# Performance work log

Measured on AMD Instinct MI355X. Metric: run time of the kernel, lower is better.

The kernel has to match this reference:

```python
import jax, jax.numpy as jnp
import numpy as np

DVEC = 128
B, S = 4, 1024


def setup_inputs() -> dict:
    key = jax.random.key(0)
    k1, k2 = jax.random.split(key)
    func_and_arg = jax.random.normal(k1, (B, S, 2 * DVEC), dtype=jnp.float32)
    cooccurrences = jax.random.normal(k2, (DVEC, DVEC, DVEC), dtype=jnp.float32)
    return {"func_and_arg": func_and_arg, "cooccurrences": cooccurrences}


def reference(func_and_arg, cooccurrences):
    # out[b,s,z] = sum_{i,j} func[b,s,i] * cooc[i,j,z] * arg[b,s,j]
    d = cooccurrences.shape[0]
    func = func_and_arg[..., :d]   # [B,S,D]
    arg = func_and_arg[..., d:]    # [B,S,D]
    # contract func over i first -> [B,S,D(j),Z], then arg over j -> [B,S,Z]
    tmp = jnp.einsum('bsi,ijz->bsjz', func, cooccurrences)
    return jnp.einsum('bsjz,bsj->bsz', tmp, arg)
```

## Files before the change

### kernel.cpp

```cpp
#include <hip/hip_runtime.h>
#include <hip/hip_bf16.h>


typedef __attribute__((ext_vector_type(8))) short bf16x8;
typedef __attribute__((ext_vector_type(4))) float f32x4;

__device__ __forceinline__ unsigned pkbf16(float x, float y) {
    __hip_bfloat162 h = __float22bfloat162_rn(make_float2(x, y));
    unsigned u; __builtin_memcpy(&u, &h, sizeof(u));
    return u;
}

__global__ __launch_bounds__(256) void cooc_transpose(
    const float* __restrict__ Cc, ushort* __restrict__ CT)
{
    __shared__ float tile[32][132];
    const int i  = blockIdx.x >> 2;
    const int j0 = (blockIdx.x & 3) * 32;
    const int t  = threadIdx.x;
    {
        const int jj = t >> 3;
        const int zb = (t & 7) * 16;
        const float* src = Cc + (size_t)i * 16384 + (size_t)(j0 + jj) * 128 + zb;
        #pragma unroll
        for (int k = 0; k < 4; ++k)
            *(float4*)&tile[jj][zb + k * 4] = *(const float4*)(src + k * 4);
    }
    __syncthreads();
    {
        const int z = t >> 1;
        const int h = t & 1;
        unsigned o[8];
        #pragma unroll
        for (int p = 0; p < 8; ++p)
            o[p] = pkbf16(tile[h * 16 + 2 * p][z], tile[h * 16 + 2 * p + 1][z]);
        const int c0 = (j0 >> 3) + h * 2;
        ushort* dst = CT + (size_t)i * 16384 + (size_t)(z >> 4) * 2048
                         + (size_t)c0 * 128 + (z & 15) * 8;
        *(uint4*)dst         = make_uint4(o[0], o[1], o[2], o[3]);
        *(uint4*)(dst + 128) = make_uint4(o[4], o[5], o[6], o[7]);
    }
}

__global__ __launch_bounds__(256) void cooc_apack(
    const float* __restrict__ fa, ushort* __restrict__ APK)
{
    const int g = blockIdx.x;
    const int t = threadIdx.x;
    const int ks = t >> 6, lk = (t >> 4) & 3, lm = t & 15;
    const float* src = fa + (size_t)(g * 16 + lm) * 256 + 128 + ks * 32 + lk * 8;
    float4 q0 = *(const float4*)src;
    float4 q1 = *(const float4*)(src + 4);
    unsigned o0 = pkbf16(q0.x, q0.y), o1 = pkbf16(q0.z, q0.w);
    unsigned o2 = pkbf16(q1.x, q1.y), o3 = pkbf16(q1.z, q1.w);
    *(uint4*)(APK + (size_t)g * 2048 + t * 8) = make_uint4(o0, o1, o2, o3);
}

template<int USE_WS>
__global__ __launch_bounds__(256, 3) void cooc_main(
    const float* __restrict__ fa, const ushort* __restrict__ CT,
    const ushort* __restrict__ APK, float* __restrict__ dst)
{
    __shared__ float f_lds[16][128];

    const int bid = blockIdx.x;
    const int kp = bid & 7, zp = (bid >> 3) & 3, mtile = bid >> 5;
    const int t0 = mtile * 128, i0 = kp * 16;
    const int tid = threadIdx.x, lane = tid & 63, wv = tid >> 6;
    const int mg = wv >> 1, zg = wv & 1;
    const int lm = lane & 15, lk = lane >> 4;

    {
        const int row = tid & 127;
        const int sh = (tid >> 7) * 8;
        const float* fp = fa + (size_t)(t0 + row) * 256 + i0 + sh;
        float4 v0 = *(const float4*)fp;
        float4 v1 = *(const float4*)(fp + 4);
        f_lds[sh + 0][row] = v0.x; f_lds[sh + 1][row] = v0.y;
        f_lds[sh + 2][row] = v0.z; f_lds[sh + 3][row] = v0.w;
        f_lds[sh + 4][row] = v1.x; f_lds[sh + 5][row] = v1.y;
        f_lds[sh + 6][row] = v1.z; f_lds[sh + 7][row] = v1.w;
    }

    bf16x8 a_pk[4][4];
    {
        const ushort* ap = APK + (size_t)((t0 >> 4) + mg * 4) * 2048 + lane * 8;
        #pragma unroll
        for (int m = 0; m < 4; ++m)
            #pragma unroll
            for (int ks = 0; ks < 4; ++ks)
                a_pk[m][ks] = *(const bf16x8*)(ap + (size_t)m * 2048 + ks * 512);
    }
    __syncthreads();

    const ushort* bsrc = CT + (size_t)i0 * 16384
                            + (size_t)(zp * 2 + zg) * 2048 + lane * 8;

    bf16x8 B[2][4];
    #pragma unroll
    for (int ks = 0; ks < 4; ++ks) {
        B[0][ks] = *(const bf16x8*)(bsrc + ks * 512);
        B[1][ks] = *(const bf16x8*)(bsrc + 16384 + ks * 512);
    }

    float acc[4][4];
    #pragma unroll
    for (int m = 0; m < 4; ++m)
        #pragma unroll
        for (int r = 0; r < 4; ++r) acc[m][r] = 0.f;

    #pragma unroll 2
    for (int s = 0; s < 16; ++s) {
        const int cur = s & 1;

        f32x4 g[4];
        #pragma unroll
        for (int m = 0; m < 4; ++m) g[m] = (f32x4){0.f, 0.f, 0.f, 0.f};
        #pragma unroll
        for (int ks = 0; ks < 4; ++ks)
            #pragma unroll
            for (int m = 0; m < 4; ++m)
                g[m] = __builtin_amdgcn_mfma_f32_16x16x32_bf16(
                    a_pk[m][ks], B[cur][ks], g[m], 0, 0, 0);

        if (s < 14) {
            const ushort* p = bsrc + (size_t)(s + 2) * 16384;
            #pragma unroll
            for (int ks = 0; ks < 4; ++ks)
                B[cur][ks] = *(const bf16x8*)(p + ks * 512);
        }

        float4 f4[4];
        #pragma unroll
        for (int m = 0; m < 4; ++m)
            f4[m] = *(const float4*)&f_lds[s][mg * 64 + m * 16 + lk * 4];
        #pragma unroll
        for (int m = 0; m < 4; ++m) {
            acc[m][0] += f4[m].x * g[m][0];
            acc[m][1] += f4[m].y * g[m][1];
            acc[m][2] += f4[m].z * g[m][2];
            acc[m][3] += f4[m].w * g[m][3];
        }
    }

    const int col = zp * 32 + zg * 16 + lm;
    #pragma unroll
    for (int m = 0; m < 4; ++m)
        #pragma unroll
        for (int r = 0; r < 4; ++r) {
            const int row = t0 + mg * 64 + m * 16 + lk * 4 + r;
            if (USE_WS)
                dst[(size_t)kp * 524288 + (size_t)row * 128 + col] = acc[m][r];
            else
                atomicAdd(&dst[(size_t)row * 128 + col], acc[m][r]);
        }
}

__global__ __launch_bounds__(256) void cooc_reduce(const float* __restrict__ ws,
                                                   float* __restrict__ out) {
    const size_t idx = ((size_t)blockIdx.x * 256 + threadIdx.x) * 4;
    float4 a = *(const float4*)(ws + idx);
    #pragma unroll
    for (int k = 1; k < 8; ++k) {
        float4 b = *(const float4*)(ws + (size_t)k * 524288 + idx);
        a.x += b.x; a.y += b.y; a.z += b.z; a.w += b.w;
    }
    *(float4*)(out + idx) = a;
}

extern "C" void kernel_launch(void* const* d_in, const int* in_sizes, int n_in,
                              void* d_out, int out_size, void* d_ws, size_t ws_size,
                              hipStream_t stream) {
    const float* fa = (const float*)d_in[0];
    const float* Cc = (const float*)d_in[1];
    float* out = (float*)d_out;

    const size_t PART = (size_t)8 * 524288;
    const size_t CTOF = PART * sizeof(float);
    const size_t CTSZ = (size_t)128 * 128 * 128 * 2;
    const size_t APOF = CTOF + CTSZ;
    const size_t APSZ = (size_t)4096 * 128 * 2;
    const size_t NEED_FULL = APOF + APSZ;
    const size_t NEED_CT   = CTSZ + APSZ;

    if (ws_size >= NEED_FULL) {
        ushort* CT  = (ushort*)((char*)d_ws + CTOF);
        ushort* APK = (ushort*)((char*)d_ws + APOF);
        cooc_transpose<<<512, 256, 0, stream>>>(Cc, CT);
        cooc_apack<<<256, 256, 0, stream>>>(fa, APK);
        cooc_main<1><<<1024, 256, 0, stream>>>(fa, CT, APK, (float*)d_ws);
        cooc_reduce<<<512, 256, 0, stream>>>((const float*)d_ws, out);
    } else if (ws_size >= NEED_CT) {
        ushort* CT  = (ushort*)d_ws;
        ushort* APK = (ushort*)((char*)d_ws + CTSZ);
        cooc_transpose<<<512, 256, 0, stream>>>(Cc, CT);
        cooc_apack<<<256, 256, 0, stream>>>(fa, APK);
        (void)hipMemsetAsync(out, 0, (size_t)out_size * sizeof(float), stream);
        cooc_main<0><<<1024, 256, 0, stream>>>(fa, CT, APK, out);
    } else {
        (void)hipMemsetAsync(out, 0, (size_t)out_size * sizeof(float), stream);
        cooc_main<0><<<1024, 256, 0, stream>>>(fa, (const ushort*)d_ws,
                                               (const ushort*)d_ws, out);
    }
}
```

Baseline: 86.22 us.

## Merge prep kernels and share cooccurrence B tiles through LDS across waves

The transpose and activation-pack kernels become a single launch, dropping one kernel launch. In the main kernel each wave now loads only half of its B chunk from global memory and the waves exchange the halves through a double-buffered LDS tile, so the two wave pairs that use the same B stop fetching it twice. The func values are stored in LDS as bf16, which halves their footprint. The cost is a __syncthreads in every iteration, extra LDS traffic, and extra rounding of func to bf16.

```diff
diff --git a/kernel.cpp b/kernel.cpp
--- a/kernel.cpp
+++ b/kernel.cpp
@@ -10,50 +10,55 @@
     unsigned u; __builtin_memcpy(&u, &h, sizeof(u));
     return u;
 }
-
-__global__ __launch_bounds__(256) void cooc_transpose(
-    const float* __restrict__ Cc, ushort* __restrict__ CT)
+__device__ __forceinline__ float bf16lo(unsigned u) {
+    unsigned v = u << 16; float f; __builtin_memcpy(&f, &v, 4); return f;
+}
+__device__ __forceinline__ float bf16hi(unsigned u) {
+    unsigned v = u & 0xFFFF0000u; float f; __builtin_memcpy(&f, &v, 4); return f;
+}
+
+__global__ __launch_bounds__(256) void cooc_prep(
+    const float* __restrict__ Cc, const float* __restrict__ fa,
+    ushort* __restrict__ CT, ushort* __restrict__ APK)
 {
-    __shared__ float tile[32][132];
-    const int i  = blockIdx.x >> 2;
-    const int j0 = (blockIdx.x & 3) * 32;
-    const int t  = threadIdx.x;
-    {
-        const int jj = t >> 3;
-        const int zb = (t & 7) * 16;
-        const float* src = Cc + (size_t)i * 16384 + (size_t)(j0 + jj) * 128 + zb;
-        #pragma unroll
-        for (int k = 0; k < 4; ++k)
-            *(float4*)&tile[jj][zb + k * 4] = *(const float4*)(src + k * 4);
-    }
-    __syncthreads();
-    {
-        const int z = t >> 1;
-        const int h = t & 1;
-        unsigned o[8];
-        #pragma unroll
-        for (int p = 0; p < 8; ++p)
-            o[p] = pkbf16(tile[h * 16 + 2 * p][z], tile[h * 16 + 2 * p + 1][z]);
-        const int c0 = (j0 >> 3) + h * 2;
-        ushort* dst = CT + (size_t)i * 16384 + (size_t)(z >> 4) * 2048
-                         + (size_t)c0 * 128 + (z & 15) * 8;
-        *(uint4*)dst         = make_uint4(o[0], o[1], o[2], o[3]);
-        *(uint4*)(dst + 128) = make_uint4(o[4], o[5], o[6], o[7]);
-    }
-}
-
-__global__ __launch_bounds__(256) void cooc_apack(
-    const float* __restrict__ fa, ushort* __restrict__ APK)
-{
-    const int g = blockIdx.x;
+    const int bid = blockIdx.x;
     const int t = threadIdx.x;
-    const int ks = t >> 6, lk = (t >> 4) & 3, lm = t & 15;
-    const float* src = fa + (size_t)(g * 16 + lm) * 256 + 128 + ks * 32 + lk * 8;
-    float4 q0 = *(const float4*)src;
-    float4 q1 = *(const float4*)(src + 4);
-    unsigned o0 = pkbf16(q0.x, q0.y), o1 = pkbf16(q0.z, q0.w);
-    unsigned o2 = pkbf16(q1.x, q1.y), o3 = pkbf16(q1.z, q1.w);
-    *(uint4*)(APK + (size_t)g * 2048 + t * 8) = make_uint4(o0, o1, o2, o3);
+    if (bid < 512) {
+        __shared__ float tile[32][132];
+        const int i  = bid >> 2;
+        const int j0 = (bid & 3) * 32;
+        {
+            const int jj = t >> 3;
+            const int zb = (t & 7) * 16;
+            const float* src = Cc + (size_t)i * 16384 + (size_t)(j0 + jj) * 128 + zb;
+            #pragma unroll
+            for (int k = 0; k < 4; ++k)
+                *(float4*)&tile[jj][zb + k * 4] = *(const float4*)(src + k * 4);
+        }
+        __syncthreads();
+        {
+            const int z = t >> 1;
+            const int h = t & 1;
+            unsigned o[8];
+            #pragma unroll
+            for (int p = 0; p < 8; ++p)
+                o[p] = pkbf16(tile[h * 16 + 2 * p][z], tile[h * 16 + 2 * p + 1][z]);
+            const int c0 = (j0 >> 3) + h * 2;
+            ushort* dst = CT + (size_t)i * 16384 + (size_t)(z >> 4) * 2048
+                             + (size_t)c0 * 128 + (z & 15) * 8;
+            *(uint4*)dst         = make_uint4(o[0], o[1], o[2], o[3]);
+            *(uint4*)(dst + 128) = make_uint4(o[4], o[5], o[6], o[7]);
+        }
+    } else {
+        const int g = bid - 512;
+        const int ks = t >> 6, lk = (t >> 4) & 3, lm = t & 15;
+        const float* src = fa + (size_t)(g * 16 + lm) * 256 + 128 + ks * 32 + lk * 8;
+        float4 q0 = *(const float4*)src;
+        float4 q1 = *(const float4*)(src + 4);
+        *(uint4*)(APK + (size_t)g * 2048 + t * 8) =
+            make_uint4(pkbf16(q0.x, q0.y), pkbf16(q0.z, q0.w),
+                       pkbf16(q1.x, q1.y), pkbf16(q1.z, q1.w));
+    }
 }
 
 template<int USE_WS>
@@ -61,7 +66,8 @@
     const float* __restrict__ fa, const ushort* __restrict__ CT,
     const ushort* __restrict__ APK, float* __restrict__ dst)
 {
-    __shared__ float f_lds[16][128];
+    __shared__ ushort Bbuf[2][2][4][512];
+    __shared__ ushort fpk[16][128];
 
     const int bid = blockIdx.x;
     const int kp = bid & 7, zp = (bid >> 3) & 3, mtile = bid >> 5;
@@ -76,10 +82,14 @@
         const float* fp = fa + (size_t)(t0 + row) * 256 + i0 + sh;
         float4 v0 = *(const float4*)fp;
         float4 v1 = *(const float4*)(fp + 4);
-        f_lds[sh + 0][row] = v0.x; f_lds[sh + 1][row] = v0.y;
-        f_lds[sh + 2][row] = v0.z; f_lds[sh + 3][row] = v0.w;
-        f_lds[sh + 4][row] = v1.x; f_lds[sh + 5][row] = v1.y;
-        f_lds[sh + 6][row] = v1.z; f_lds[sh + 7][row] = v1.w;
+        fpk[sh + 0][row] = (ushort)(pkbf16(v0.x, v0.x) & 0xFFFF);
+        fpk[sh + 1][row] = (ushort)(pkbf16(v0.y, v0.y) & 0xFFFF);
+        fpk[sh + 2][row] = (ushort)(pkbf16(v0.z, v0.z) & 0xFFFF);
+        fpk[sh + 3][row] = (ushort)(pkbf16(v0.w, v0.w) & 0xFFFF);
+        fpk[sh + 4][row] = (ushort)(pkbf16(v1.x, v1.x) & 0xFFFF);
+        fpk[sh + 5][row] = (ushort)(pkbf16(v1.y, v1.y) & 0xFFFF);
+        fpk[sh + 6][row] = (ushort)(pkbf16(v1.z, v1.z) & 0xFFFF);
+        fpk[sh + 7][row] = (ushort)(pkbf16(v1.w, v1.w) & 0xFFFF);
     }
 
     bf16x8 a_pk[4][4];
@@ -91,17 +101,21 @@
             for (int ks = 0; ks < 4; ++ks)
                 a_pk[m][ks] = *(const bf16x8*)(ap + (size_t)m * 2048 + ks * 512);
     }
+
+    const ushort* bchunk = CT + (size_t)i0 * 16384
+                              + (size_t)(zp * 2 + zg) * 2048
+                              + (size_t)(2 * mg) * 512 + lane * 8;
+
+    bf16x8 Bg[2][2];
+    #pragma unroll
+    for (int c = 0; c < 2; ++c) {
+        Bg[0][c] = *(const bf16x8*)(bchunk + c * 512);
+        Bg[1][c] = *(const bf16x8*)(bchunk + 16384 + c * 512);
+    }
+    #pragma unroll
+    for (int c = 0; c < 2; ++c)
+        *(bf16x8*)&Bbuf[0][zg][2 * mg + c][lane * 8] = Bg[0][c];
     __syncthreads();
-
-    const ushort* bsrc = CT + (size_t)i0 * 16384
-                            + (size_t)(zp * 2 + zg) * 2048 + lane * 8;
-
-    bf16x8 B[2][4];
-    #pragma unroll
-    for (int ks = 0; ks < 4; ++ks) {
-        B[0][ks] = *(const bf16x8*)(bsrc + ks * 512);
-        B[1][ks] = *(const bf16x8*)(bsrc + 16384 + ks * 512);
-    }
 
     float acc[4][4];
     #pragma unroll
@@ -113,6 +127,28 @@
     for (int s = 0; s < 16; ++s) {
         const int cur = s & 1;
 
+        if (s < 15)
+            #pragma unroll
+            for (int c = 0; c < 2; ++c)
+                *(bf16x8*)&Bbuf[cur ^ 1][zg][2 * mg + c][lane * 8] = Bg[cur ^ 1][c];
+
+        if (s < 14) {
+            const ushort* p = bchunk + (size_t)(s + 2) * 16384;
+            #pragma unroll
+            for (int c = 0; c < 2; ++c)
+                Bg[cur][c] = *(const bf16x8*)(p + c * 512);
+        }
+
+        bf16x8 Bl[4];
+        #pragma unroll
+        for (int ks = 0; ks < 4; ++ks)
+            Bl[ks] = *(const bf16x8*)&Bbuf[cur][zg][ks][lane * 8];
+
+        uint2 fq[4];
+        #pragma unroll
+        for (int m = 0; m < 4; ++m)
+            fq[m] = *(const uint2*)&fpk[s][mg * 64 + m * 16 + lk * 4];
+
         f32x4 g[4];
         #pragma unroll
         for (int m = 0; m < 4; ++m) g[m] = (f32x4){0.f, 0.f, 0.f, 0.f};
@@ -121,26 +157,17 @@
             #pragma unroll
             for (int m = 0; m < 4; ++m)
                 g[m] = __builtin_amdgcn_mfma_f32_16x16x32_bf16(
-                    a_pk[m][ks], B[cur][ks], g[m], 0, 0, 0);
-
-        if (s < 14) {
-            const ushort* p = bsrc + (size_t)(s + 2) * 16384;
-            #pragma unroll
-            for (int ks = 0; ks < 4; ++ks)
-                B[cur][ks] = *(const bf16x8*)(p + ks * 512);
-        }
-
-        float4 f4[4];
-        #pragma unroll
-        for (int m = 0; m < 4; ++m)
-            f4[m] = *(const float4*)&f_lds[s][mg * 64 + m * 16 + lk * 4];
+                    a_pk[m][ks], Bl[ks], g[m], 0, 0, 0);
+
         #pragma unroll
         for (int m = 0; m < 4; ++m) {
-            acc[m][0] += f4[m].x * g[m][0];
-            acc[m][1] += f4[m].y * g[m][1];
-            acc[m][2] += f4[m].z * g[m][2];
-            acc[m][3] += f4[m].w * g[m][3];
-        }
+            acc[m][0] += bf16lo(fq[m].x) * g[m][0];
+            acc[m][1] += bf16hi(fq[m].x) * g[m][1];
+            acc[m][2] += bf16lo(fq[m].y) * g[m][2];
+            acc[m][3] += bf16hi(fq[m].y) * g[m][3];
+        }
+
+        __syncthreads();
     }
 
     const int col = zp * 32 + zg * 16 + lm;
@@ -186,15 +213,13 @@
     if (ws_size >= NEED_FULL) {
         ushort* CT  = (ushort*)((char*)d_ws + CTOF);
         ushort* APK = (ushort*)((char*)d_ws + APOF);
-        cooc_transpose<<<512, 256, 0, stream>>>(Cc, CT);
-        cooc_apack<<<256, 256, 0, stream>>>(fa, APK);
+        cooc_prep<<<768, 256, 0, stream>>>(Cc, fa, CT, APK);
         cooc_main<1><<<1024, 256, 0, stream>>>(fa, CT, APK, (float*)d_ws);
         cooc_reduce<<<512, 256, 0, stream>>>((const float*)d_ws, out);
     } else if (ws_size >= NEED_CT) {
         ushort* CT  = (ushort*)d_ws;
         ushort* APK = (ushort*)((char*)d_ws + CTSZ);
-        cooc_transpose<<<512, 256, 0, stream>>>(Cc, CT);
-        cooc_apack<<<256, 256, 0, stream>>>(fa, APK);
+        cooc_prep<<<768, 256, 0, stream>>>(Cc, fa, CT, APK);
         (void)hipMemsetAsync(out, 0, (size_t)out_size * sizeof(float), stream);
         cooc_main<0><<<1024, 256, 0, stream>>>(fa, CT, APK, out);
     } else {
```

After: 86.18 us. No clear change (-0.0%).

## Merge prep kernels and halve main-kernel M tile to double grid size

Applied to the files above, without the earlier changes.

Folds the cooc transpose and A-packing kernels into one launch, with the work chosen by block index, which removes one kernel launch. The main kernel's row tile drops from 128 to 64, so the grid doubles to 2048 blocks, the register and LDS footprint per block shrinks, and the occupancy hint rises from 3 to 4 blocks. In exchange, each B tile loaded from CT now feeds half as many MFMAs, so the CT operand is re-read twice as often across the grid. The a_pk array also gains a redundant copy that is never read.

```diff
diff --git a/kernel.cpp b/kernel.cpp
--- a/kernel.cpp
+++ b/kernel.cpp
@@ -11,85 +11,85 @@
     return u;
 }
 
-__global__ __launch_bounds__(256) void cooc_transpose(
-    const float* __restrict__ Cc, ushort* __restrict__ CT)
+__global__ __launch_bounds__(256) void cooc_prep(
+    const float* __restrict__ Cc, const float* __restrict__ fa,
+    ushort* __restrict__ CT, ushort* __restrict__ APK)
 {
-    __shared__ float tile[32][132];
-    const int i  = blockIdx.x >> 2;
-    const int j0 = (blockIdx.x & 3) * 32;
-    const int t  = threadIdx.x;
-    {
-        const int jj = t >> 3;
-        const int zb = (t & 7) * 16;
-        const float* src = Cc + (size_t)i * 16384 + (size_t)(j0 + jj) * 128 + zb;
-        #pragma unroll
-        for (int k = 0; k < 4; ++k)
-            *(float4*)&tile[jj][zb + k * 4] = *(const float4*)(src + k * 4);
-    }
-    __syncthreads();
-    {
-        const int z = t >> 1;
-        const int h = t & 1;
-        unsigned o[8];
-        #pragma unroll
-        for (int p = 0; p < 8; ++p)
-            o[p] = pkbf16(tile[h * 16 + 2 * p][z], tile[h * 16 + 2 * p + 1][z]);
-        const int c0 = (j0 >> 3) + h * 2;
-        ushort* dst = CT + (size_t)i * 16384 + (size_t)(z >> 4) * 2048
-                         + (size_t)c0 * 128 + (z & 15) * 8;
-        *(uint4*)dst         = make_uint4(o[0], o[1], o[2], o[3]);
-        *(uint4*)(dst + 128) = make_uint4(o[4], o[5], o[6], o[7]);
-    }
-}
-
-__global__ __launch_bounds__(256) void cooc_apack(
-    const float* __restrict__ fa, ushort* __restrict__ APK)
-{
-    const int g = blockIdx.x;
+    const int bid = blockIdx.x;
     const int t = threadIdx.x;
-    const int ks = t >> 6, lk = (t >> 4) & 3, lm = t & 15;
-    const float* src = fa + (size_t)(g * 16 + lm) * 256 + 128 + ks * 32 + lk * 8;
-    float4 q0 = *(const float4*)src;
-    float4 q1 = *(const float4*)(src + 4);
-    unsigned o0 = pkbf16(q0.x, q0.y), o1 = pkbf16(q0.z, q0.w);
-    unsigned o2 = pkbf16(q1.x, q1.y), o3 = pkbf16(q1.z, q1.w);
-    *(uint4*)(APK + (size_t)g * 2048 + t * 8) = make_uint4(o0, o1, o2, o3);
+    if (bid < 512) {
+        __shared__ float tile[32][132];
+        const int i  = bid >> 2;
+        const int j0 = (bid & 3) * 32;
+        {
+            const int jj = t >> 3;
+            const int zb = (t & 7) * 16;
+            const float* src = Cc + (size_t)i * 16384 + (size_t)(j0 + jj) * 128 + zb;
+            #pragma unroll
+            for (int k = 0; k < 4; ++k)
+                *(float4*)&tile[jj][zb + k * 4] = *(const float4*)(src + k * 4);
+        }
+        __syncthreads();
+        {
+            const int z = t >> 1;
+            const int h = t & 1;
+            unsigned o[8];
+            #pragma unroll
+            for (int p = 0; p < 8; ++p)
+                o[p] = pkbf16(tile[h * 16 + 2 * p][z], tile[h * 16 + 2 * p + 1][z]);
+            const int c0 = (j0 >> 3) + h * 2;
+            ushort* dst = CT + (size_t)i * 16384 + (size_t)(z >> 4) * 2048
+                             + (size_t)c0 * 128 + (z & 15) * 8;
+            *(uint4*)dst         = make_uint4(o[0], o[1], o[2], o[3]);
+            *(uint4*)(dst + 128) = make_uint4(o[4], o[5], o[6], o[7]);
+        }
+    } else {
+        const int g = bid - 512;
+        const int ks = t >> 6, lk = (t >> 4) & 3, lm = t & 15;
+        const float* src = fa + (size_t)(g * 16 + lm) * 256 + 128 + ks * 32 + lk * 8;
+        float4 q0 = *(const float4*)src;
+        float4 q1 = *(const float4*)(src + 4);
+        *(uint4*)(APK + (size_t)g * 2048 + t * 8) =
+            make_uint4(pkbf16(q0.x, q0.y), pkbf16(q0.z, q0.w),
+                       pkbf16(q1.x, q1.y), pkbf16(q1.z, q1.w));
+    }
 }
 
 template<int USE_WS>
-__global__ __launch_bounds__(256, 3) void cooc_main(
+__global__ __launch_bounds__(256, 4) void cooc_main(
     const float* __restrict__ fa, const ushort* __restrict__ CT,
     const ushort* __restrict__ APK, float* __restrict__ dst)
 {
-    __shared__ float f_lds[16][128];
+    __shared__ float f_lds[16][64];
 
     const int bid = blockIdx.x;
     const int kp = bid & 7, zp = (bid >> 3) & 3, mtile = bid >> 5;
-    const int t0 = mtile * 128, i0 = kp * 16;
+    const int t0 = mtile * 64, i0 = kp * 16;
     const int tid = threadIdx.x, lane = tid & 63, wv = tid >> 6;
     const int mg = wv >> 1, zg = wv & 1;
     const int lm = lane & 15, lk = lane >> 4;
 
     {
-        const int row = tid & 127;
-        const int sh = (tid >> 7) * 8;
+        const int row = tid & 63;
+        const int sh = (tid >> 6) * 4;
         const float* fp = fa + (size_t)(t0 + row) * 256 + i0 + sh;
-        float4 v0 = *(const float4*)fp;
-        float4 v1 = *(const float4*)(fp + 4);
-        f_lds[sh + 0][row] = v0.x; f_lds[sh + 1][row] = v0.y;
-        f_lds[sh + 2][row] = v0.z; f_lds[sh + 3][row] = v0.w;
-        f_lds[sh + 4][row] = v1.x; f_lds[sh + 5][row] = v1.y;
-        f_lds[sh + 6][row] = v1.z; f_lds[sh + 7][row] = v1.w;
-    }
-
-    bf16x8 a_pk[4][4];
+        float4 v = *(const float4*)fp;
+        f_lds[sh + 0][row] = v.x;
+        f_lds[sh + 1][row] = v.y;
+        f_lds[sh + 2][row] = v.z;
+        f_lds[sh + 3][row] = v.w;
+    }
+
+    bf16x8 a_pk[2][2][4];
     {
-        const ushort* ap = APK + (size_t)((t0 >> 4) + mg * 4) * 2048 + lane * 8;
-        #pragma unroll
-        for (int m = 0; m < 4; ++m)
-            #pragma unroll
-            for (int ks = 0; ks < 4; ++ks)
-                a_pk[m][ks] = *(const bf16x8*)(ap + (size_t)m * 2048 + ks * 512);
+        const ushort* ap = APK + (size_t)((t0 >> 4) + mg * 2) * 2048 + lane * 8;
+        #pragma unroll
+        for (int m = 0; m < 2; ++m)
+            #pragma unroll
+            for (int ks = 0; ks < 4; ++ks) {
+                a_pk[0][m][ks] = *(const bf16x8*)(ap + (size_t)m * 2048 + ks * 512);
+                a_pk[1][m][ks] = a_pk[0][m][ks];
+            }
     }
     __syncthreads();
 
@@ -103,9 +103,9 @@
         B[1][ks] = *(const bf16x8*)(bsrc + 16384 + ks * 512);
     }
 
-    float acc[4][4];
-    #pragma unroll
-    for (int m = 0; m < 4; ++m)
+    float acc[2][4];
+    #pragma unroll
+    for (int m = 0; m < 2; ++m)
         #pragma unroll
         for (int r = 0; r < 4; ++r) acc[m][r] = 0.f;
 
@@ -113,15 +113,16 @@
     for (int s = 0; s < 16; ++s) {
         const int cur = s & 1;
 
-        f32x4 g[4];
-        #pragma unroll
-        for (int m = 0; m < 4; ++m) g[m] = (f32x4){0.f, 0.f, 0.f, 0.f};
-        #pragma unroll
-        for (int ks = 0; ks < 4; ++ks)
-            #pragma unroll
-            for (int m = 0; m < 4; ++m)
-                g[m] = __builtin_amdgcn_mfma_f32_16x16x32_bf16(
-                    a_pk[m][ks], B[cur][ks], g[m], 0, 0, 0);
+        f32x4 g[2];
+        g[0] = (f32x4){0.f, 0.f, 0.f, 0.f};
+        g[1] = (f32x4){0.f, 0.f, 0.f, 0.f};
+        #pragma unroll
+        for (int ks = 0; ks < 4; ++ks) {
+            g[0] = __builtin_amdgcn_mfma_f32_16x16x32_bf16(
+                a_pk[0][0][ks], B[cur][ks], g[0], 0, 0, 0);
+            g[1] = __builtin_amdgcn_mfma_f32_16x16x32_bf16(
+                a_pk[0][1][ks], B[cur][ks], g[1], 0, 0, 0);
+        }
 
         if (s < 14) {
             const ushort* p = bsrc + (size_t)(s + 2) * 16384;
@@ -130,12 +131,11 @@
                 B[cur][ks] = *(const bf16x8*)(p + ks * 512);
         }
 
-        float4 f4[4];
-        #pragma unroll
-        for (int m = 0; m < 4; ++m)
-            f4[m] = *(const float4*)&f_lds[s][mg * 64 + m * 16 + lk * 4];
-        #pragma unroll
-        for (int m = 0; m < 4; ++m) {
+        float4 f4[2];
+        f4[0] = *(const float4*)&f_lds[s][mg * 32 + lk * 4];
+        f4[1] = *(const float4*)&f_lds[s][mg * 32 + 16 + lk * 4];
+        #pragma unroll
+        for (int m = 0; m < 2; ++m) {
             acc[m][0] += f4[m].x * g[m][0];
             acc[m][1] += f4[m].y * g[m][1];
             acc[m][2] += f4[m].z * g[m][2];
@@ -145,10 +145,10 @@
 
     const int col = zp * 32 + zg * 16 + lm;
     #pragma unroll
-    for (int m = 0; m < 4; ++m)
+    for (int m = 0; m < 2; ++m)
         #pragma unroll
         for (int r = 0; r < 4; ++r) {
-            const int row = t0 + mg * 64 + m * 16 + lk * 4 + r;
+            const int row = t0 + mg * 32 + m * 16 + lk * 4 + r;
             if (USE_WS)
                 dst[(size_t)kp * 524288 + (size_t)row * 128 + col] = acc[m][r];
             else
@@ -186,20 +186,18 @@
     if (ws_size >= NEED_FULL) {
         ushort* CT  = (ushort*)((char*)d_ws + CTOF);
         ushort* APK = (ushort*)((char*)d_ws + APOF);
-        cooc_transpose<<<512, 256, 0, stream>>>(Cc, CT);
-        cooc_apack<<<256, 256, 0, stream>>>(fa, APK);
-        cooc_main<1><<<1024, 256, 0, stream>>>(fa, CT, APK, (float*)d_ws);
+        cooc_prep<<<768, 256, 0, stream>>>(Cc, fa, CT, APK);
+        cooc_main<1><<<2048, 256, 0, stream>>>(fa, CT, APK, (float*)d_ws);
         cooc_reduce<<<512, 256, 0, stream>>>((const float*)d_ws, out);
     } else if (ws_size >= NEED_CT) {
         ushort* CT  = (ushort*)d_ws;
         ushort* APK = (ushort*)((char*)d_ws + CTSZ);
-        cooc_transpose<<<512, 256, 0, stream>>>(Cc, CT);
-        cooc_apack<<<256, 256, 0, stream>>>(fa, APK);
+        cooc_prep<<<768, 256, 0, stream>>>(Cc, fa, CT, APK);
         (void)hipMemsetAsync(out, 0, (size_t)out_size * sizeof(float), stream);
-        cooc_main<0><<<1024, 256, 0, stream>>>(fa, CT, APK, out);
+        cooc_main<0><<<2048, 256, 0, stream>>>(fa, CT, APK, out);
     } else {
         (void)hipMemsetAsync(out, 0, (size_t)out_size * sizeof(float), stream);
-        cooc_main<0><<<1024, 256, 0, stream>>>(fa, (const ushort*)d_ws,
+        cooc_main<0><<<2048, 256, 0, stream>>>(fa, (const ushort*)d_ws,
                                                (const ushort*)d_ws, out);
     }
 }
```

Measured after the change: 89.00 us. 1.03x slower.

## Fuse prep kernels and output zeroing, replace workspace reduction with atomics

Applied to the files above, without the earlier changes.

Merges the bf16 transpose of the cooccurrence tensor, the arg packing, and zeroing of the output into one launch. The main kernel now always accumulates its 8 K-split partials with atomicAdd, which removes the partial-sum workspace and the separate reduce kernel. The aim is fewer kernel launches and less workspace traffic, at the cost of atomic contention on the output and a non-deterministic summation order. A naive fp32 fallback replaces the old path for a too-small workspace.

```diff
diff --git a/kernel.cpp b/kernel.cpp
--- a/kernel.cpp
+++ b/kernel.cpp
@@ -11,55 +11,60 @@
     return u;
 }
 
-__global__ __launch_bounds__(256) void cooc_transpose(
-    const float* __restrict__ Cc, ushort* __restrict__ CT)
+__global__ __launch_bounds__(256) void cooc_prep(
+    const float* __restrict__ Cc, const float* __restrict__ fa,
+    ushort* __restrict__ CT, ushort* __restrict__ APK, float* __restrict__ out)
 {
-    __shared__ float tile[32][132];
-    const int i  = blockIdx.x >> 2;
-    const int j0 = (blockIdx.x & 3) * 32;
-    const int t  = threadIdx.x;
-    {
-        const int jj = t >> 3;
-        const int zb = (t & 7) * 16;
-        const float* src = Cc + (size_t)i * 16384 + (size_t)(j0 + jj) * 128 + zb;
+    const int bid = blockIdx.x;
+    const int t = threadIdx.x;
+    if (bid < 512) {
+        __shared__ float tile[32][132];
+        const int i  = bid >> 2;
+        const int j0 = (bid & 3) * 32;
+        {
+            const int jj = t >> 3;
+            const int zb = (t & 7) * 16;
+            const float* src = Cc + (size_t)i * 16384 + (size_t)(j0 + jj) * 128 + zb;
+            #pragma unroll
+            for (int k = 0; k < 4; ++k)
+                *(float4*)&tile[jj][zb + k * 4] = *(const float4*)(src + k * 4);
+        }
+        __syncthreads();
+        {
+            const int z = t >> 1;
+            const int h = t & 1;
+            unsigned o[8];
+            #pragma unroll
+            for (int p = 0; p < 8; ++p)
+                o[p] = pkbf16(tile[h * 16 + 2 * p][z], tile[h * 16 + 2 * p + 1][z]);
+            const int c0 = (j0 >> 3) + h * 2;
+            ushort* dst = CT + (size_t)i * 16384 + (size_t)(z >> 4) * 2048
+                             + (size_t)c0 * 128 + (z & 15) * 8;
+            *(uint4*)dst         = make_uint4(o[0], o[1], o[2], o[3]);
+            *(uint4*)(dst + 128) = make_uint4(o[4], o[5], o[6], o[7]);
+        }
+    } else if (bid < 768) {
+        const int g = bid - 512;
+        const int ks = t >> 6, lk = (t >> 4) & 3, lm = t & 15;
+        const float* src = fa + (size_t)(g * 16 + lm) * 256 + 128 + ks * 32 + lk * 8;
+        float4 q0 = *(const float4*)src;
+        float4 q1 = *(const float4*)(src + 4);
+        *(uint4*)(APK + (size_t)g * 2048 + t * 8) =
+            make_uint4(pkbf16(q0.x, q0.y), pkbf16(q0.z, q0.w),
+                       pkbf16(q1.x, q1.y), pkbf16(q1.z, q1.w));
+    } else {
+        float4* o4 = (float4*)out;
+        const size_t base = (size_t)(bid - 768) * 256 + t;
+        const float4 z4 = {0.f, 0.f, 0.f, 0.f};
         #pragma unroll
-        for (int k = 0; k < 4; ++k)
-            *(float4*)&tile[jj][zb + k * 4] = *(const float4*)(src + k * 4);
-    }
-    __syncthreads();
-    {
-        const int z = t >> 1;
-        const int h = t & 1;
-        unsigned o[8];
-        #pragma unroll
-        for (int p = 0; p < 8; ++p)
-            o[p] = pkbf16(tile[h * 16 + 2 * p][z], tile[h * 16 + 2 * p + 1][z]);
-        const int c0 = (j0 >> 3) + h * 2;
-        ushort* dst = CT + (size_t)i * 16384 + (size_t)(z >> 4) * 2048
-                         + (size_t)c0 * 128 + (z & 15) * 8;
-        *(uint4*)dst         = make_uint4(o[0], o[1], o[2], o[3]);
-        *(uint4*)(dst + 128) = make_uint4(o[4], o[5], o[6], o[7]);
+        for (int k = 0; k < 64; ++k)
+            o4[base + (size_t)k * 2048] = z4;
     }
 }
 
-__global__ __launch_bounds__(256) void cooc_apack(
-    const float* __restrict__ fa, ushort* __restrict__ APK)
-{
-    const int g = blockIdx.x;
-    const int t = threadIdx.x;
-    const int ks = t >> 6, lk = (t >> 4) & 3, lm = t & 15;
-    const float* src = fa + (size_t)(g * 16 + lm) * 256 + 128 + ks * 32 + lk * 8;
-    float4 q0 = *(const float4*)src;
-    float4 q1 = *(const float4*)(src + 4);
-    unsigned o0 = pkbf16(q0.x, q0.y), o1 = pkbf16(q0.z, q0.w);
-    unsigned o2 = pkbf16(q1.x, q1.y), o3 = pkbf16(q1.z, q1.w);
-    *(uint4*)(APK + (size_t)g * 2048 + t * 8) = make_uint4(o0, o1, o2, o3);
-}
-
-template<int USE_WS>
 __global__ __launch_bounds__(256, 3) void cooc_main(
     const float* __restrict__ fa, const ushort* __restrict__ CT,
-    const ushort* __restrict__ APK, float* __restrict__ dst)
+    const ushort* __restrict__ APK, float* __restrict__ out)
 {
     __shared__ float f_lds[16][128];
 
@@ -149,23 +154,27 @@
         #pragma unroll
         for (int r = 0; r < 4; ++r) {
             const int row = t0 + mg * 64 + m * 16 + lk * 4 + r;
-            if (USE_WS)
-                dst[(size_t)kp * 524288 + (size_t)row * 128 + col] = acc[m][r];
-            else
-                atomicAdd(&dst[(size_t)row * 128 + col], acc[m][r]);
+            atomicAdd(&out[(size_t)row * 128 + col], acc[m][r]);
         }
 }
 
-__global__ __launch_bounds__(256) void cooc_reduce(const float* __restrict__ ws,
-                                                   float* __restrict__ out) {
-    const size_t idx = ((size_t)blockIdx.x * 256 + threadIdx.x) * 4;
-    float4 a = *(const float4*)(ws + idx);
-    #pragma unroll
-    for (int k = 1; k < 8; ++k) {
-        float4 b = *(const float4*)(ws + (size_t)k * 524288 + idx);
-        a.x += b.x; a.y += b.y; a.z += b.z; a.w += b.w;
+__global__ __launch_bounds__(128) void cooc_naive(
+    const float* __restrict__ fa, const float* __restrict__ Cc,
+    float* __restrict__ out)
+{
+    const int tk = blockIdx.x;
+    const int z  = threadIdx.x;
+    const float* f = fa + (size_t)tk * 256;
+    const float* a = f + 128;
+    float s = 0.f;
+    for (int i = 0; i < 128; ++i) {
+        const float fi = f[i];
+        const float* cr = Cc + (size_t)i * 16384 + z;
+        float t = 0.f;
+        for (int j = 0; j < 128; ++j) t += a[j] * cr[(size_t)j * 128];
+        s += fi * t;
     }
-    *(float4*)(out + idx) = a;
+    out[(size_t)tk * 128 + z] = s;
 }
 
 extern "C" void kernel_launch(void* const* d_in, const int* in_sizes, int n_in,
@@ -175,31 +184,15 @@
     const float* Cc = (const float*)d_in[1];
     float* out = (float*)d_out;
 
-    const size_t PART = (size_t)8 * 524288;
-    const size_t CTOF = PART * sizeof(float);
     const size_t CTSZ = (size_t)128 * 128 * 128 * 2;
-    const size_t APOF = CTOF + CTSZ;
     const size_t APSZ = (size_t)4096 * 128 * 2;
-    const size_t NEED_FULL = APOF + APSZ;
-    const size_t NEED_CT   = CTSZ + APSZ;
 
-    if (ws_size >= NEED_FULL) {
-        ushort* CT  = (ushort*)((char*)d_ws + CTOF);
-        ushort* APK = (ushort*)((char*)d_ws + APOF);
-        cooc_transpose<<<512, 256, 0, stream>>>(Cc, CT);
-        cooc_apack<<<256, 256, 0, stream>>>(fa, APK);
-        cooc_main<1><<<1024, 256, 0, stream>>>(fa, CT, APK, (float*)d_ws);
-        cooc_reduce<<<512, 256, 0, stream>>>((const float*)d_ws, out);
-    } else if (ws_size >= NEED_CT) {
+    if (ws_size >= CTSZ + APSZ) {
         ushort* CT  = (ushort*)d_ws;
         ushort* APK = (ushort*)((char*)d_ws + CTSZ);
-        cooc_transpose<<<512, 256, 0, stream>>>(Cc, CT);
-        cooc_apack<<<256, 256, 0, stream>>>(fa, APK);
-        (void)hipMemsetAsync(out, 0, (size_t)out_size * sizeof(float), stream);
-        cooc_main<0><<<1024, 256, 0, stream>>>(fa, CT, APK, out);
+        cooc_prep<<<776, 256, 0, stream>>>(Cc, fa, CT, APK, out);
+        cooc_main<<<1024, 256, 0, stream>>>(fa, CT, APK, out);
     } else {
-        (void)hipMemsetAsync(out, 0, (size_t)out_size * sizeof(float), stream);
-        cooc_main<0><<<1024, 256, 0, stream>>>(fa, (const ushort*)d_ws,
-                                               (const ushort*)d_ws, out);
+        cooc_naive<<<4096, 128, 0, stream>>>(fa, Cc, out);
     }
 }
```

Result: slower. 89.32 us (+3.6%).
